# Optimization experiments

Measured on AMD Instinct MI355X. Metric: run time of the kernel, lower is better.

## Reference

```python
import jax, jax.numpy as jnp
import numpy as np


def _to_box_list(x):
    # (batch, ch, nw, nh) -> (nw*nh, batch, ch)  [convert_to_box_list]
    b, c, nw, nh = x.shape
    return jnp.transpose(x, (2, 3, 0, 1)).reshape(nw * nh, b, c)


def _bilinear_sample(img, px, py):
    # img: (ch, X, Y); px: (Sx,), py: (Sy,) pixel coords; zero padding outside.
    ch, X, Y = img.shape
    x0 = jnp.floor(px); y0 = jnp.floor(py)
    wx = px - x0; wy = py - y0
    x0i = x0.astype(jnp.int32); y0i = y0.astype(jnp.int32)
    def g(xi, yi):
        xc = jnp.clip(xi, 0, X - 1); yc = jnp.clip(yi, 0, Y - 1)
        v = img[:, xc[:, None], yc[None, :]]
        m = (((xi >= 0) & (xi < X))[:, None] & ((yi >= 0) & (yi < Y))[None, :]).astype(img.dtype)
        return v * m
    return ((1 - wx)[:, None] * ((1 - wy)[None, :] * g(x0i, y0i) + wy[None, :] * g(x0i, y0i + 1))
            + wx[:, None] * ((1 - wy)[None, :] * g(x0i + 1, y0i) + wy[None, :] * g(x0i + 1, y0i + 1)))


def setup_inputs():
    key = jax.random.key(0)
    ks = jax.random.split(key, 12)
    B, CH_IN, W, H = 8, 1, 256, 256
    NW = NH = 32
    DZW, DZI, FCH, S = 4, 16, 32, 28
    feat_flat = FCH * S * S   # 25088
    out_flat = (CH_IN + 1) * S * S  # 1568
    return {
        "imgs_in": jax.random.uniform(ks[0], (B, CH_IN, W, H), jnp.float32),
        "features": jax.random.normal(ks[1], (B, FCH, W, H), jnp.float32),
        "zwhere_mu": jax.random.normal(ks[2], (B, DZW, NW, NH), jnp.float32),
        "zwhere_std": jax.random.uniform(ks[3], (B, DZW, NW, NH), jnp.float32) * 0.9 + 0.1,
        "logit_mu": jax.random.normal(ks[4], (B, 1, NW, NH), jnp.float32),
        "w_zwhere": jax.random.normal(ks[5], (4, DZW), jnp.float32) * 0.5,
        "b_zwhere": jnp.zeros((4,), jnp.float32),
        "w_enc_mu": jax.random.normal(ks[6], (DZI, feat_flat), jnp.float32) * 0.01,
        "b_enc_mu": jnp.zeros((DZI,), jnp.float32),
        "w_enc_std": jax.random.normal(ks[7], (DZI, feat_flat), jnp.float32) * 0.01,
        "b_enc_std": jnp.zeros((DZI,), jnp.float32),
        "w_dec": jax.random.normal(ks[8], (out_flat, DZI), jnp.float32) * 0.1,
        "b_dec": jnp.zeros((out_flat,), jnp.float32),
        "n_objects_max": 25,
        "cropped_size": 28,
        "size_min": 24,
        "size_max": 96,
    }


def reference(imgs_in, features, zwhere_mu, zwhere_std, logit_mu,
              w_zwhere, b_zwhere, w_enc_mu, b_enc_mu, w_enc_std, b_enc_std,
              w_dec, b_dec, n_objects_max, cropped_size, size_min, size_max):
    B, CH_IN, W, H = imgs_in.shape
    S = cropped_size
    eps = 1e-8

    # ---- box decode: Decoder1by1Linear (1x1 conv) + sigmoid + tmaps_to_bb ----
    tmaps = jax.nn.sigmoid(jnp.einsum('bcwh,oc->bowh', zwhere_mu, w_zwhere)
                           + b_zwhere[None, :, None, None])
    tx, ty, tw, th = tmaps[:, 0], tmaps[:, 1], tmaps[:, 2], tmaps[:, 3]  # (B, nw, nh)
    nw, nh = tx.shape[-2], tx.shape[-1]
    ix = jnp.arange(nw, dtype=tx.dtype)[:, None]
    iy = jnp.arange(nh, dtype=tx.dtype)[None, :]
    def tolist2(m):  # (B, nw, nh) -> (nw*nh, B)
        return jnp.transpose(m, (1, 2, 0)).reshape(nw * nh, B)
    bx_all = tolist2(W * (ix + tx) / nw)
    by_all = tolist2(H * (iy + ty) / nh)
    bw_all = tolist2(size_min + (size_max - size_min) * tw)
    bh_all = tolist2(size_min + (size_max - size_min) * th)

    # ---- prob map, Bernoulli KL vs prior 0.5, deterministic top-k (topk_only NMS) ----
    p_map = jax.nn.sigmoid(logit_mu)                                     # c_map.sample
    kl_logit = (jnp.log(2.0) + p_map * jnp.log(p_map + eps)
                + (1 - p_map) * jnp.log(1 - p_map + eps))               # c_map.kl
    p_list = _to_box_list(p_map)[..., 0]        # (n_all, B)
    logit_list = _to_box_list(logit_mu)[..., 0]
    _, idx_bk = jax.lax.top_k(p_list.T, n_objects_max)  # (B, k)
    index_top_k = idx_bk.T                              # (k, B)

    c_few = jnp.take_along_axis(p_list, index_top_k, axis=0)
    logit_few = jnp.take_along_axis(logit_list, index_top_k, axis=0)
    bx = jnp.take_along_axis(bx_all, index_top_k, axis=0)
    by = jnp.take_along_axis(by_all, index_top_k, axis=0)
    bw = jnp.take_along_axis(bw_all, index_top_k, axis=0)
    bh = jnp.take_along_axis(bh_all, index_top_k, axis=0)

    # ---- zwhere KL (diag normal vs N(0,1)), gathered at top-k boxes ----
    kl_zwhere_map = 0.5 * (zwhere_std ** 2 + zwhere_mu ** 2 - 1.0) - jnp.log(zwhere_std)
    kl_zwhere_all = _to_box_list(kl_zwhere_map)          # (n_all, B, dz)
    idx3 = jnp.broadcast_to(index_top_k[:, :, None],
                            (n_objects_max, B, kl_zwhere_all.shape[-1]))
    kl_zwhere_few = jnp.take_along_axis(kl_zwhere_all, idx3, axis=0)

    # ---- Cropper.crop: bilinear crop of UNet features at selected boxes ----
    def crop_one(img, cx, cy, cw, chh):
        t = jnp.arange(S, dtype=img.dtype) / (S - 1)
        return _bilinear_sample(img, cx - 0.5 * cw + t * cw, cy - 0.5 * chh + t * chh)
    crop_boxes = jax.vmap(crop_one, in_axes=(None, 0, 0, 0, 0))
    crop_all = jax.vmap(crop_boxes, in_axes=(0, 1, 1, 1, 1), out_axes=1)
    cropped = crop_all(features, bx, by, bw, bh)  # (k, B, FCH, S, S)

    # ---- encoder_zinstance -> z sample (= mu, noisy_sampling=False) + KL ----
    xf = cropped.reshape(n_objects_max, B, -1)
    z_mu = xf @ w_enc_mu.T + b_enc_mu
    z_std = jax.nn.softplus(xf @ w_enc_std.T + b_enc_std)
    z_sample = z_mu
    kl_zinstance = 0.5 * (z_std ** 2 + z_mu ** 2 - 1.0) - jnp.log(z_std + eps)

    # ---- decoder_zinstance -> small stuff: softplus weight ch, sigmoid img ch ----
    small_raw = (z_sample @ w_dec.T + b_dec).reshape(n_objects_max, B, CH_IN + 1, S, S)
    small = jnp.concatenate([jax.nn.softplus(small_raw[..., :1, :, :]),
                             jax.nn.sigmoid(small_raw[..., 1:, :, :])], axis=-3)

    # ---- Uncropper.uncrop: paste each small patch back at its box location ----
    def uncrop_one(sm, cx, cy, cw, chh):
        u = jnp.arange(W, dtype=sm.dtype)
        v = jnp.arange(H, dtype=sm.dtype)
        sx = (u - (cx - 0.5 * cw)) / cw * (S - 1)
        sy = (v - (cy - 0.5 * chh)) / chh * (S - 1)
        return _bilinear_sample(sm, sx, sy)
    big_stuff = jax.vmap(jax.vmap(uncrop_one))(small, bx, by, bw, bh)  # (k,B,2,W,H)

    big_weight = big_stuff[..., :1, :, :]
    big_img = big_stuff[..., 1:, :, :]
    sum_w = jnp.sum(big_weight, axis=0, keepdims=True)  # dim=-5 is box dim
    big_mask = jnp.tanh(sum_w) * (big_weight / jnp.clip(sum_w, 1e-6))
    big_mask_non = jnp.tanh(big_weight)

    return (logit_mu, logit_few, big_mask, big_mask_non, big_img,
            p_map, c_few, bx, by, bw, bh, z_sample,
            kl_logit, kl_zwhere_few, kl_zinstance)
```

## Files before the change

kernel.cpp:

```cpp
#include <hip/hip_runtime.h>
#include <math.h>

#define B 8
#define FCH 32
#define WI 256
#define HI 256
#define NW 32
#define NH 32
#define NBOX 1024
#define K 25
#define S 28
#define DZI 16
#define FEAT_FLAT (FCH*S*S)
#define FEAT4 (FEAT_FLAT/4)
#define OUT_FLAT (2*S*S)
#define SMIN 24.0f
#define SMAX 96.0f
#define BIG_SZ (K*B*WI*HI)

#define NCHUNK 49
#define CH4 128

#define O_LOGIT_MU    0
#define O_LOGIT_FEW   8192
#define O_BIG_MASK    8392
#define O_BIG_MASK_NON (O_BIG_MASK + BIG_SZ)
#define O_BIG_IMG     (O_BIG_MASK_NON + BIG_SZ)
#define O_P_MAP       (O_BIG_IMG + BIG_SZ)
#define O_C_FEW       (O_P_MAP + 8192)
#define O_BX          (O_C_FEW + 200)
#define O_BY          (O_BX + 200)
#define O_BW          (O_BY + 200)
#define O_BH          (O_BW + 200)
#define O_Z_SAMPLE    (O_BH + 200)
#define O_KL_LOGIT    (O_Z_SAMPLE + 3200)
#define O_KL_ZWHERE   (O_KL_LOGIT + 8192)
#define O_KL_ZINST    (O_KL_ZWHERE + 800)

__device__ __forceinline__ float sigmoidf_(float x) { return 1.0f / (1.0f + expf(-x)); }
__device__ __forceinline__ float softplusf_(float x) { return fmaxf(x, 0.0f) + log1pf(expf(-fabsf(x))); }
__device__ __forceinline__ float sig_fast(float x) { return 1.0f / (1.0f + __expf(-x)); }
__device__ __forceinline__ float sp_fast(float x)  { return fmaxf(x, 0.0f) + __logf(1.0f + __expf(-fabsf(x))); }
__device__ __forceinline__ float tanh_fast(float x) {
    float e = __expf(-2.0f * x);
    return (1.0f - e) / (1.0f + e);
}

__device__ __forceinline__ float tap256(const float* img, int x, int y) {
    bool in = ((unsigned)x < 256u) && ((unsigned)y < 256u);
    int xc = min(max(x, 0), 255), yc = min(max(y, 0), 255);
    float v = img[xc * 256 + yc];
    return in ? v : 0.0f;
}

__device__ __forceinline__ float tap28(const float* img, int x, int y) {
    bool in = ((unsigned)x < 28u) && ((unsigned)y < 28u);
    int xc = min(max(x, 0), 27), yc = min(max(y, 0), 27);
    float v = img[xc * 28 + yc];
    return in ? v : 0.0f;
}

__global__ void topk_misc_kernel(const float* __restrict__ logit_mu,
                                 const float* __restrict__ zmu, const float* __restrict__ zstd,
                                 const float* __restrict__ w_zw, const float* __restrict__ b_zw,
                                 float* __restrict__ out, float* __restrict__ ws_boxes) {
    int b = blockIdx.x;
    int lane = threadIdx.x;
    const float* lg = logit_mu + b * NBOX;
    float vals[16];
    #pragma unroll
    for (int m = 0; m < 16; ++m) vals[m] = lg[m * 64 + lane];

    #pragma unroll
    for (int m = 0; m < 16; ++m) {
        int idx = b * NBOX + m * 64 + lane;
        float x = vals[m];
        out[O_LOGIT_MU + idx] = x;
        float p = sigmoidf_(x);
        out[O_P_MAP + idx] = p;
        out[O_KL_LOGIT + idx] = 0.69314718055994531f + p * logf(p + 1e-8f) + (1.0f - p) * logf(1.0f - p + 1e-8f);
    }

    unsigned taken = 0;
    int sel_idx = 0;
    for (int ks = 0; ks < K; ++ks) {
        float bv = -INFINITY; int bi = 0x7fffffff;
        #pragma unroll
        for (int m = 0; m < 16; ++m) {
            if (!(taken & (1u << m))) {
                float v = vals[m]; int idx = m * 64 + lane;
                if (v > bv || (v == bv && idx < bi)) { bv = v; bi = idx; }
            }
        }
        #pragma unroll
        for (int sh = 32; sh >= 1; sh >>= 1) {
            float ov = __shfl_xor(bv, sh);
            int   oi = __shfl_xor(bi, sh);
            if (ov > bv || (ov == bv && oi < bi)) { bv = ov; bi = oi; }
        }
        if ((bi & 63) == lane) taken |= (1u << (bi >> 6));
        if (lane == ks) sel_idx = bi;
        if (lane == 0) {
            out[O_LOGIT_FEW + ks * B + b] = bv;
            out[O_C_FEW + ks * B + b] = sigmoidf_(bv);
        }
    }

    if (lane < K) {
        int idx = sel_idx;
        int w = idx >> 5, h = idx & 31;
        float mu_c[4];
        #pragma unroll
        for (int c = 0; c < 4; ++c) mu_c[c] = zmu[((b * 4 + c) * NW + w) * NH + h];
        float t[4];
        #pragma unroll
        for (int o = 0; o < 4; ++o) {
            float a = b_zw[o];
            #pragma unroll
            for (int c = 0; c < 4; ++c) a = fmaf(mu_c[c], w_zw[o * 4 + c], a);
            t[o] = sigmoidf_(a);
        }
        float bx = (float)WI * ((float)w + t[0]) / (float)NW;
        float by = (float)HI * ((float)h + t[1]) / (float)NH;
        float bw = SMIN + (SMAX - SMIN) * t[2];
        float bh = SMIN + (SMAX - SMIN) * t[3];
        int kb = lane * B + b;
        out[O_BX + kb] = bx;
        out[O_BY + kb] = by;
        out[O_BW + kb] = bw;
        out[O_BH + kb] = bh;
        ((float4*)ws_boxes)[kb] = make_float4(bx, by, bw, bh);
        #pragma unroll
        for (int c = 0; c < 4; ++c) {
            float m = mu_c[c];
            float sd = zstd[((b * 4 + c) * NW + w) * NH + h];
            out[O_KL_ZWHERE + kb * 4 + c] = 0.5f * (sd * sd + m * m - 1.0f) - logf(sd);
        }
    }
}

__global__ __launch_bounds__(256) void crop_writer_kernel(
        const float* __restrict__ features, const float* __restrict__ ws_boxes,
        float* __restrict__ crop) {
    int c  = blockIdx.x;
    int kb = blockIdx.y;
    int b  = kb & 7;
    float4 box = ((const float4*)ws_boxes)[kb];
    float x_lo = box.x - 0.5f * box.z, y_lo = box.y - 0.5f * box.w;
    float swx = box.z * (1.0f / 27.0f), swy = box.w * (1.0f / 27.0f);
    const float* img = features + ((size_t)b * FCH + c) * (WI * HI);
    float* dst = crop + (size_t)kb * FEAT_FLAT + c * 784;

    int wave = threadIdx.x >> 6, lane = threadIdx.x & 63;
    int h  = lane >> 5;
    int iy = lane & 31;
    if (iy < 28) {
        float py = fmaf((float)iy, swy, y_lo);
        float y0f = floorf(py);
        float fy = py - y0f;
        int y0 = (int)y0f;
        for (int p = wave; p < 14; p += 4) {
            int ix = 2 * p + h;
            float px = fmaf((float)ix, swx, x_lo);
            float x0f = floorf(px);
            float fx = px - x0f;
            int x0 = (int)x0f;
            float a00 = tap256(img, x0, y0),     a01 = tap256(img, x0, y0 + 1);
            float a10 = tap256(img, x0 + 1, y0), a11 = tap256(img, x0 + 1, y0 + 1);
            float v = (1.0f - fx) * ((1.0f - fy) * a00 + fy * a01)
                    +         fx  * ((1.0f - fy) * a10 + fy * a11);
            dst[ix * 28 + iy] = v;
        }
    }
}

__device__ __forceinline__ float dot4f(float4 v, float4 w, float a) {
    return fmaf(v.x, w.x, fmaf(v.y, w.y, fmaf(v.z, w.z, fmaf(v.w, w.w, a))));
}

__global__ __launch_bounds__(512) void enc_gemm_kernel(
        const float* __restrict__ crop,
        const float* __restrict__ w_mu, const float* __restrict__ w_std,
        float* __restrict__ ws_part) {
    int blk = blockIdx.x;
    int g = blk / NCHUNK, chunk = blk - g * NCHUNK;
    int wave = threadIdx.x >> 6, lane = threadIdx.x & 63;
    int base4 = chunk * CH4;
    const float4* cp4 = (const float4*)crop;

    __shared__ float4 crop_lds[8][CH4];
    {
        int t1 = threadIdx.x, t2 = threadIdx.x + 512;
        crop_lds[t1 >> 7][t1 & 127] = cp4[(size_t)(g * 8 + (t1 >> 7)) * FEAT4 + base4 + (t1 & 127)];
        crop_lds[t2 >> 7][t2 & 127] = cp4[(size_t)(g * 8 + (t2 >> 7)) * FEAT4 + base4 + (t2 & 127)];
    }

    int row = wave * 4;
    const float4* wsrc = (row < 16) ? ((const float4*)w_mu + (size_t)row * FEAT4)
                                    : ((const float4*)w_std + (size_t)(row - 16) * FEAT4);
    int i4a = base4 + lane, i4b = i4a + 64;
    float4 wa[4], wb[4];
    #pragma unroll
    for (int r = 0; r < 4; ++r) {
        wa[r] = wsrc[(size_t)r * FEAT4 + i4a];
        wb[r] = wsrc[(size_t)r * FEAT4 + i4b];
    }

    float cur[32];
    #pragma unroll
    for (int j = 0; j < 32; ++j) cur[j] = 0.0f;

    __syncthreads();

    #pragma unroll
    for (int bb = 0; bb < 8; ++bb) {
        float4 ca = crop_lds[bb][lane];
        float4 cb = crop_lds[bb][lane + 64];
        #pragma unroll
        for (int r = 0; r < 4; ++r)
            cur[r * 8 + bb] = dot4f(cb, wb[r], dot4f(ca, wa[r], cur[r * 8 + bb]));
    }

    {   bool bit = (lane & 1) != 0; float nx[16];
        #pragma unroll
        for (int j = 0; j < 16; ++j) {
            float keep = bit ? cur[2*j+1] : cur[2*j];
            float send = bit ? cur[2*j]   : cur[2*j+1];
            nx[j] = keep + __shfl_xor(send, 1);
        }
        #pragma unroll
        for (int j = 0; j < 16; ++j) cur[j] = nx[j];
    }
    {   bool bit = (lane & 2) != 0; float nx[8];
        #pragma unroll
        for (int j = 0; j < 8; ++j) {
            float keep = bit ? cur[2*j+1] : cur[2*j];
            float send = bit ? cur[2*j]   : cur[2*j+1];
            nx[j] = keep + __shfl_xor(send, 2);
        }
        #pragma unroll
        for (int j = 0; j < 8; ++j) cur[j] = nx[j];
    }
    {   bool bit = (lane & 4) != 0; float nx[4];
        #pragma unroll
        for (int j = 0; j < 4; ++j) {
            float keep = bit ? cur[2*j+1] : cur[2*j];
            float send = bit ? cur[2*j]   : cur[2*j+1];
            nx[j] = keep + __shfl_xor(send, 4);
        }
        #pragma unroll
        for (int j = 0; j < 4; ++j) cur[j] = nx[j];
    }
    {   bool bit = (lane & 8) != 0; float nx[2];
        #pragma unroll
        for (int j = 0; j < 2; ++j) {
            float keep = bit ? cur[2*j+1] : cur[2*j];
            float send = bit ? cur[2*j]   : cur[2*j+1];
            nx[j] = keep + __shfl_xor(send, 8);
        }
        cur[0] = nx[0]; cur[1] = nx[1];
    }
    {   bool bit = (lane & 16) != 0;
        float keep = bit ? cur[1] : cur[0];
        float send = bit ? cur[0] : cur[1];
        cur[0] = keep + __shfl_xor(send, 16);
    }
    float tot = cur[0] + __shfl_xor(cur[0], 32);
    if (lane < 32) {
        int kbx = g * 8 + (lane & 7);
        ws_part[((size_t)kbx * NCHUNK + chunk) * 32 + row + (lane >> 3)] = tot;
    }
}

__global__ __launch_bounds__(256) void dec_enc_kernel(
        const float* __restrict__ ws_part,
        const float* __restrict__ b_mu, const float* __restrict__ b_std,
        const float* __restrict__ w_dec, const float* __restrict__ b_dec,
        float* __restrict__ ws_small, float* __restrict__ out) {
    int kb = blockIdx.x;
    int t = threadIdx.x;
    __shared__ float zsh[DZI], spsh[DZI];
    if (t < 32) {
        float s = 0.0f;
        for (int c = 0; c < NCHUNK; ++c) s += ws_part[((size_t)kb * NCHUNK + c) * 32 + t];
        if (t < DZI) zsh[t] = s + b_mu[t];
        else         spsh[t - DZI] = s + b_std[t - DZI];
    }
    __syncthreads();
    if (t < DZI) {
        float m = zsh[t];
        float sd = softplusf_(spsh[t]);
        out[O_Z_SAMPLE + kb * DZI + t] = m;
        out[O_KL_ZINST + kb * DZI + t] = 0.5f * (sd * sd + m * m - 1.0f) - logf(sd + 1e-8f);
    }
    float z[DZI];
    #pragma unroll
    for (int j = 0; j < DZI; ++j) z[j] = zsh[j];
    for (int o = t; o < OUT_FLAT; o += 256) {
        const float4* wd = (const float4*)(w_dec + o * DZI);
        float4 w0 = wd[0], w1 = wd[1], w2 = wd[2], w3 = wd[3];
        float a = b_dec[o];
        a = fmaf(z[0], w0.x, fmaf(z[1], w0.y, fmaf(z[2], w0.z, fmaf(z[3], w0.w, a))));
        a = fmaf(z[4], w1.x, fmaf(z[5], w1.y, fmaf(z[6], w1.z, fmaf(z[7], w1.w, a))));
        a = fmaf(z[8], w2.x, fmaf(z[9], w2.y, fmaf(z[10], w2.z, fmaf(z[11], w2.w, a))));
        a = fmaf(z[12], w3.x, fmaf(z[13], w3.y, fmaf(z[14], w3.z, fmaf(z[15], w3.w, a))));
        float r = (o < 784) ? sp_fast(a) : sig_fast(a);
        ws_small[(size_t)kb * OUT_FLAT + o] = r;
    }
}

__device__ __forceinline__ void sample2_wi(const float* __restrict__ p0, float sx,
                                           float y_lo, float ih, int v0,
                                           float* __restrict__ w, float* __restrict__ im) {
    const float* p1 = p0 + 784;
    float x0f = floorf(sx); float fx = sx - x0f; int x0 = (int)x0f;
    #pragma unroll
    for (int q = 0; q < 2; ++q) {
        float sy = ((float)(v0 + q) - y_lo) * ih;
        float wv = 0.0f, iv = 0.0f;
        if (sy > -1.0f && sy < 28.0f) {
            float y0f = floorf(sy); float fy = sy - y0f; int y0 = (int)y0f;
            float a00 = tap28(p0, x0, y0),     a01 = tap28(p0, x0, y0 + 1);
            float a10 = tap28(p0, x0 + 1, y0), a11 = tap28(p0, x0 + 1, y0 + 1);
            wv = (1.0f - fx) * ((1.0f - fy) * a00 + fy * a01)
               +         fx  * ((1.0f - fy) * a10 + fy * a11);
            float c00 = tap28(p1, x0, y0),     c01 = tap28(p1, x0, y0 + 1);
            float c10 = tap28(p1, x0 + 1, y0), c11 = tap28(p1, x0 + 1, y0 + 1);
            iv = (1.0f - fx) * ((1.0f - fy) * c00 + fy * c01)
               +         fx  * ((1.0f - fy) * c10 + fy * c11);
        }
        w[q] = wv; im[q] = iv;
    }
}

__device__ __forceinline__ void sample2_w(const float* __restrict__ p0, float sx,
                                          float y_lo, float ih, int v0,
                                          float* __restrict__ w) {
    float x0f = floorf(sx); float fx = sx - x0f; int x0 = (int)x0f;
    #pragma unroll
    for (int q = 0; q < 2; ++q) {
        float sy = ((float)(v0 + q) - y_lo) * ih;
        float wv = 0.0f;
        if (sy > -1.0f && sy < 28.0f) {
            float y0f = floorf(sy); float fy = sy - y0f; int y0 = (int)y0f;
            float a00 = tap28(p0, x0, y0),     a01 = tap28(p0, x0, y0 + 1);
            float a10 = tap28(p0, x0 + 1, y0), a11 = tap28(p0, x0 + 1, y0 + 1);
            wv = (1.0f - fx) * ((1.0f - fy) * a00 + fy * a01)
               +         fx  * ((1.0f - fy) * a10 + fy * a11);
        }
        w[q] = wv;
    }
}

__global__ __launch_bounds__(256) void uncrop_kernel(const float* __restrict__ ws_small,
                                                     const float* __restrict__ ws_boxes,
                                                     float* __restrict__ out) {
    int blk = blockIdx.x;
    int b = blk >> 7;
    int ug = blk & 127;
    int t = threadIdx.x;
    int u = ug * 2 + (t >> 7);
    int v0 = (t & 127) << 1;

    __shared__ float4 bt[K];
    if (t < K) {
        float4 bx = ((const float4*)ws_boxes)[t * B + b];
        bt[t] = make_float4(bx.x - 0.5f * bx.z, bx.y - 0.5f * bx.w, 27.0f / bx.z, 27.0f / bx.w);
    }
    __syncthreads();

    float fu = (float)u;
    float sum[2] = {0.0f, 0.0f};
    #pragma unroll 2
    for (int k = 0; k < K; ++k) {
        float4 bb = bt[k];
        float sx = (fu - bb.x) * bb.z;
        float w[2] = {0, 0}, im[2] = {0, 0};
        if (sx > -1.0f && sx < 28.0f) {
            const float* p0 = ws_small + (size_t)(k * B + b) * OUT_FLAT;
            sample2_wi(p0, sx, bb.y, bb.w, v0, w, im);
        }
        sum[0] += w[0]; sum[1] += w[1];
        size_t base = (((size_t)(k * B + b) * 256 + u) * 256 + v0);
        *(float2*)(out + O_BIG_IMG + base) = make_float2(im[0], im[1]);
        *(float2*)(out + O_BIG_MASK_NON + base) = make_float2(tanh_fast(w[0]), tanh_fast(w[1]));
    }
    float sc[2];
    sc[0] = tanh_fast(sum[0]) / fmaxf(sum[0], 1e-6f);
    sc[1] = tanh_fast(sum[1]) / fmaxf(sum[1], 1e-6f);
    #pragma unroll 2
    for (int k = 0; k < K; ++k) {
        float4 bb = bt[k];
        float sx = (fu - bb.x) * bb.z;
        float w[2] = {0, 0};
        if (sx > -1.0f && sx < 28.0f) {
            const float* p0 = ws_small + (size_t)(k * B + b) * OUT_FLAT;
            sample2_w(p0, sx, bb.y, bb.w, v0, w);
        }
        size_t base = (((size_t)(k * B + b) * 256 + u) * 256 + v0);
        *(float2*)(out + O_BIG_MASK + base) = make_float2(w[0] * sc[0], w[1] * sc[1]);
    }
}

extern "C" void kernel_launch(void* const* d_in, const int* in_sizes, int n_in,
                              void* d_out, int out_size, void* d_ws, size_t ws_size,
                              hipStream_t stream) {
    const float* features = (const float*)d_in[1];
    const float* zwhere_mu = (const float*)d_in[2];
    const float* zwhere_std = (const float*)d_in[3];
    const float* logit_mu = (const float*)d_in[4];
    const float* w_zwhere = (const float*)d_in[5];
    const float* b_zwhere = (const float*)d_in[6];
    const float* w_enc_mu = (const float*)d_in[7];
    const float* b_enc_mu = (const float*)d_in[8];
    const float* w_enc_std = (const float*)d_in[9];
    const float* b_enc_std = (const float*)d_in[10];
    const float* w_dec = (const float*)d_in[11];
    const float* b_dec = (const float*)d_in[12];
    float* out = (float*)d_out;

    float* ws_boxes = (float*)d_ws;
    float* ws_part  = ws_boxes + 200 * 4;
    float* ws_small = ws_part + 200 * NCHUNK * 32;
    float* ws_crop  = out + O_BIG_IMG;

    hipLaunchKernelGGL(topk_misc_kernel, dim3(B), dim3(64), 0, stream,
                       logit_mu, zwhere_mu, zwhere_std, w_zwhere, b_zwhere, out, ws_boxes);
    hipLaunchKernelGGL(crop_writer_kernel, dim3(FCH, 200), dim3(256), 0, stream,
                       features, ws_boxes, ws_crop);
    hipLaunchKernelGGL(enc_gemm_kernel, dim3(25 * NCHUNK), dim3(512), 0, stream,
                       ws_crop, w_enc_mu, w_enc_std, ws_part);
    hipLaunchKernelGGL(dec_enc_kernel, dim3(K * B), dim3(256), 0, stream,
                       ws_part, b_enc_mu, b_enc_std, w_dec, b_dec, ws_small, out);
    hipLaunchKernelGGL(uncrop_kernel, dim3(B * 128), dim3(256), 0, stream,
                       ws_small, ws_boxes, out);
}
```

Before: 111.3 us.

## Batch crop gathers, move logit elementwise work, use nontemporal big stores

Three separate changes. The crop writer now issues all bilinear tap loads for up to four rows before doing any interpolation, which raises memory-level parallelism. The per-pixel logit, p_map and KL outputs move out of the serial top-k kernel into 32 extra blocks of the decoder kernel, which shortens the top-k critical path. The large uncrop outputs are written with nontemporal stores to reduce cache pollution, at some risk of changing store coalescing behaviour.

```diff
diff --git a/kernel.cpp b/kernel.cpp
--- a/kernel.cpp
+++ b/kernel.cpp
@@ -21,6 +21,8 @@
 #define NCHUNK 49
 #define CH4 128
 
+typedef float v2f __attribute__((ext_vector_type(2)));
+
 #define O_LOGIT_MU    0
 #define O_LOGIT_FEW   8192
 #define O_BIG_MASK    8392
@@ -60,26 +62,16 @@
     return in ? v : 0.0f;
 }
 
-__global__ void topk_misc_kernel(const float* __restrict__ logit_mu,
-                                 const float* __restrict__ zmu, const float* __restrict__ zstd,
-                                 const float* __restrict__ w_zw, const float* __restrict__ b_zw,
-                                 float* __restrict__ out, float* __restrict__ ws_boxes) {
+__global__ void topk_kernel(const float* __restrict__ logit_mu,
+                            const float* __restrict__ zmu, const float* __restrict__ zstd,
+                            const float* __restrict__ w_zw, const float* __restrict__ b_zw,
+                            float* __restrict__ out, float* __restrict__ ws_boxes) {
     int b = blockIdx.x;
     int lane = threadIdx.x;
     const float* lg = logit_mu + b * NBOX;
     float vals[16];
     #pragma unroll
     for (int m = 0; m < 16; ++m) vals[m] = lg[m * 64 + lane];
-
-    #pragma unroll
-    for (int m = 0; m < 16; ++m) {
-        int idx = b * NBOX + m * 64 + lane;
-        float x = vals[m];
-        out[O_LOGIT_MU + idx] = x;
-        float p = sigmoidf_(x);
-        out[O_P_MAP + idx] = p;
-        out[O_KL_LOGIT + idx] = 0.69314718055994531f + p * logf(p + 1e-8f) + (1.0f - p) * logf(1.0f - p + 1e-8f);
-    }
 
     unsigned taken = 0;
     int sel_idx = 0;
@@ -154,22 +146,37 @@
     int wave = threadIdx.x >> 6, lane = threadIdx.x & 63;
     int h  = lane >> 5;
     int iy = lane & 31;
-    if (iy < 28) {
-        float py = fmaf((float)iy, swy, y_lo);
-        float y0f = floorf(py);
-        float fy = py - y0f;
-        int y0 = (int)y0f;
-        for (int p = wave; p < 14; p += 4) {
-            int ix = 2 * p + h;
-            float px = fmaf((float)ix, swx, x_lo);
-            float x0f = floorf(px);
-            float fx = px - x0f;
-            int x0 = (int)x0f;
-            float a00 = tap256(img, x0, y0),     a01 = tap256(img, x0, y0 + 1);
-            float a10 = tap256(img, x0 + 1, y0), a11 = tap256(img, x0 + 1, y0 + 1);
-            float v = (1.0f - fx) * ((1.0f - fy) * a00 + fy * a01)
-                    +         fx  * ((1.0f - fy) * a10 + fy * a11);
-            dst[ix * 28 + iy] = v;
+    if (iy >= 28) return;
+
+    float py = fmaf((float)iy, swy, y_lo);
+    float y0f = floorf(py);
+    float fy = py - y0f;
+    int y0 = (int)y0f;
+    int nits = (wave < 2) ? 4 : 3;
+
+    float A00[4], A01[4], A10[4], A11[4], FX[4];
+    int IX[4];
+    #pragma unroll
+    for (int it = 0; it < 4; ++it) {
+        int p = wave + it * 4;
+        int ix = (it < nits) ? (2 * p + h) : h;
+        IX[it] = ix;
+        float px = fmaf((float)ix, swx, x_lo);
+        float x0f = floorf(px);
+        FX[it] = px - x0f;
+        int x0 = (int)x0f;
+        A00[it] = tap256(img, x0, y0);
+        A01[it] = tap256(img, x0, y0 + 1);
+        A10[it] = tap256(img, x0 + 1, y0);
+        A11[it] = tap256(img, x0 + 1, y0 + 1);
+    }
+    #pragma unroll
+    for (int it = 0; it < 4; ++it) {
+        if (it < nits) {
+            float fx = FX[it];
+            float v = (1.0f - fx) * ((1.0f - fy) * A00[it] + fy * A01[it])
+                    +         fx  * ((1.0f - fy) * A10[it] + fy * A11[it]);
+            dst[IX[it] * 28 + iy] = v;
         }
     }
 }
@@ -276,9 +283,19 @@
         const float* __restrict__ ws_part,
         const float* __restrict__ b_mu, const float* __restrict__ b_std,
         const float* __restrict__ w_dec, const float* __restrict__ b_dec,
+        const float* __restrict__ logit_mu,
         float* __restrict__ ws_small, float* __restrict__ out) {
     int kb = blockIdx.x;
     int t = threadIdx.x;
+    if (kb >= K * B) {
+        int i = (kb - K * B) * 256 + t;
+        float x = logit_mu[i];
+        out[O_LOGIT_MU + i] = x;
+        float p = sigmoidf_(x);
+        out[O_P_MAP + i] = p;
+        out[O_KL_LOGIT + i] = 0.69314718055994531f + p * logf(p + 1e-8f) + (1.0f - p) * logf(1.0f - p + 1e-8f);
+        return;
+    }
     __shared__ float zsh[DZI], spsh[DZI];
     if (t < 32) {
         float s = 0.0f;
@@ -307,6 +324,11 @@
         float r = (o < 784) ? sp_fast(a) : sig_fast(a);
         ws_small[(size_t)kb * OUT_FLAT + o] = r;
     }
+}
+
+__device__ __forceinline__ void nt_store2(float* p, float a, float b) {
+    v2f v = { a, b };
+    __builtin_nontemporal_store(v, (v2f*)p);
 }
 
 __device__ __forceinline__ void sample2_wi(const float* __restrict__ p0, float sx,
@@ -382,8 +404,8 @@
         }
         sum[0] += w[0]; sum[1] += w[1];
         size_t base = (((size_t)(k * B + b) * 256 + u) * 256 + v0);
-        *(float2*)(out + O_BIG_IMG + base) = make_float2(im[0], im[1]);
-        *(float2*)(out + O_BIG_MASK_NON + base) = make_float2(tanh_fast(w[0]), tanh_fast(w[1]));
+        nt_store2(out + O_BIG_IMG + base, im[0], im[1]);
+        nt_store2(out + O_BIG_MASK_NON + base, tanh_fast(w[0]), tanh_fast(w[1]));
     }
     float sc[2];
     sc[0] = tanh_fast(sum[0]) / fmaxf(sum[0], 1e-6f);
@@ -398,7 +420,7 @@
             sample2_w(p0, sx, bb.y, bb.w, v0, w);
         }
         size_t base = (((size_t)(k * B + b) * 256 + u) * 256 + v0);
-        *(float2*)(out + O_BIG_MASK + base) = make_float2(w[0] * sc[0], w[1] * sc[1]);
+        nt_store2(out + O_BIG_MASK + base, w[0] * sc[0], w[1] * sc[1]);
     }
 }
 
@@ -424,14 +446,14 @@
     float* ws_small = ws_part + 200 * NCHUNK * 32;
     float* ws_crop  = out + O_BIG_IMG;
 
-    hipLaunchKernelGGL(topk_misc_kernel, dim3(B), dim3(64), 0, stream,
+    hipLaunchKernelGGL(topk_kernel, dim3(B), dim3(64), 0, stream,
                        logit_mu, zwhere_mu, zwhere_std, w_zwhere, b_zwhere, out, ws_boxes);
     hipLaunchKernelGGL(crop_writer_kernel, dim3(FCH, 200), dim3(256), 0, stream,
                        features, ws_boxes, ws_crop);
     hipLaunchKernelGGL(enc_gemm_kernel, dim3(25 * NCHUNK), dim3(512), 0, stream,
                        ws_crop, w_enc_mu, w_enc_std, ws_part);
-    hipLaunchKernelGGL(dec_enc_kernel, dim3(K * B), dim3(256), 0, stream,
-                       ws_part, b_enc_mu, b_enc_std, w_dec, b_dec, ws_small, out);
+    hipLaunchKernelGGL(dec_enc_kernel, dim3(K * B + 32), dim3(256), 0, stream,
+                       ws_part, b_enc_mu, b_enc_std, w_dec, b_dec, logit_mu, ws_small, out);
     hipLaunchKernelGGL(uncrop_kernel, dim3(B * 128), dim3(256), 0, stream,
                        ws_small, ws_boxes, out);
 }
```

Measured after the change: 138.3 us. 24.3% more time.
